# Kernel tuning notes

Measured on AMD Instinct MI355X. Metric: run time of the kernel, lower is better.

Reference implementation:

```python
import jax, jax.numpy as jnp
import numpy as np

N, B, D, H, E = 1024, 8, 768, 8, 16384
DH = D // H
EPS = 1e-5


def setup_inputs() -> dict:
    key = jax.random.key(0)
    ks = jax.random.split(key, 12)
    s = 0.02
    return {
        "x": jax.random.normal(ks[0], (N, B, D), jnp.float32),
        "edge_index": jax.random.randint(ks[1], (B, 2, E), 0, N, jnp.int32),
        "gcn_W": jax.random.normal(ks[2], (D, D), jnp.float32) * s,
        "gcn_b": jnp.zeros((D,), jnp.float32),
        "in_proj_w": jax.random.normal(ks[3], (3 * D, D), jnp.float32) * s,
        "in_proj_b": jnp.zeros((3 * D,), jnp.float32),
        "out_proj_w": jax.random.normal(ks[4], (D, D), jnp.float32) * s,
        "out_proj_b": jnp.zeros((D,), jnp.float32),
        "gate_w": jax.random.normal(ks[5], (D, 2 * D), jnp.float32) * s,
        "gate_b": jnp.zeros((D,), jnp.float32),
        "ln_g": jnp.ones((D,), jnp.float32),
        "ln_b": jnp.zeros((D,), jnp.float32),
    }


def _gcn(xb, edge_index, gcn_W, gcn_b):
    # xb: [B, N, D] node features; edge_index: [B, 2, E]
    h = xb @ gcn_W.T  # linear first, as in PyG GCNConv
    loops = jnp.arange(N, dtype=edge_index.dtype)

    def agg(h_b, ei_b):
        src = jnp.concatenate([ei_b[0], loops])  # add self-loops
        dst = jnp.concatenate([ei_b[1], loops])
        deg = jax.ops.segment_sum(jnp.ones_like(src, h_b.dtype), dst, num_segments=N)
        dinv = jnp.where(deg > 0, jax.lax.rsqrt(deg), 0.0)
        norm = dinv[src] * dinv[dst]  # symmetric normalization
        msg = norm[:, None] * h_b[src]
        return jax.ops.segment_sum(msg, dst, num_segments=N)

    return jax.vmap(agg)(h, edge_index) + gcn_b  # [B, N, D]


def _mha(x, in_proj_w, in_proj_b, out_proj_w, out_proj_b):
    # x: [N, B, D] (seq-first, as nn.MultiheadAttention default)
    qkv = x @ in_proj_w.T + in_proj_b  # [N, B, 3D]
    q, k, v = jnp.split(qkv, 3, axis=-1)

    def heads(t):  # [N, B, D] -> [B, H, N, DH]
        return t.reshape(N, B, H, DH).transpose(1, 2, 0, 3)

    q, k, v = heads(q), heads(k), heads(v)
    scores = jnp.einsum("bhqd,bhkd->bhqk", q, k) / jnp.sqrt(jnp.float32(DH))
    attn = jax.nn.softmax(scores, axis=-1)
    ctx = jnp.einsum("bhqk,bhkd->bhqd", attn, v)  # [B, H, N, DH]
    ctx = ctx.transpose(2, 0, 1, 3).reshape(N, B, D)
    return ctx @ out_proj_w.T + out_proj_b


def _layernorm(x, g, b):
    mu = jnp.mean(x, axis=-1, keepdims=True)
    var = jnp.mean(jnp.square(x - mu), axis=-1, keepdims=True)
    return (x - mu) * jax.lax.rsqrt(var + EPS) * g + b


def reference(x, edge_index, gcn_W, gcn_b, in_proj_w, in_proj_b,
              out_proj_w, out_proj_b, gate_w, gate_b, ln_g, ln_b):
    xb = x.transpose(1, 0, 2)  # [B, N, D]
    gcn_out = _gcn(xb, edge_index, gcn_W, gcn_b).transpose(1, 0, 2)  # [N, B, D]
    attn_out = _mha(x, in_proj_w, in_proj_b, out_proj_w, out_proj_b)  # [N, B, D]
    combined = jnp.concatenate([gcn_out, attn_out], axis=-1)
    gate = jax.nn.sigmoid(combined @ gate_w.T + gate_b)
    fused = gate * gcn_out + (1.0 - gate) * attn_out
    return _layernorm(fused + x, ln_g, ln_b)
```

## Files before the change

kernel.cpp:

```cpp
#include <hip/hip_runtime.h>


typedef __attribute__((ext_vector_type(8))) short b16x8;
typedef __attribute__((ext_vector_type(4))) float f32x4;

using gu32 = __attribute__((address_space(1))) const unsigned int;
using lu32 = __attribute__((address_space(3))) unsigned int;

constexpr int N  = 1024;
constexpr int B  = 8;
constexpr int D  = 768;
constexpr int H  = 8;
constexpr int DH = 96;
constexpr int E  = 16384;
constexpr int M  = N * B;
constexpr float LN_EPS = 1e-5f;

#define DEV static __device__ __forceinline__
#define GLOAD(SRC, DST) __builtin_amdgcn_global_load_lds((gu32*)(SRC), (lu32*)(DST), 16, 0, 0)

DEV unsigned short f2b(float f) {
  unsigned u = __float_as_uint(f);
  u += 0x7fffu + ((u >> 16) & 1u);
  return (unsigned short)(u >> 16);
}
DEV float b2f(unsigned short h) { return __uint_as_float(((unsigned)h) << 16); }

constexpr int CS0 = 1572864;
constexpr int CS1 = CS0 + 147456;
constexpr int CS2 = CS1 + 442368;
constexpr int CS3 = CS2 + 147456;
constexpr int CS4 = CS3 + 294912;
constexpr int CAST_BLOCKS = CS4 / 256;
constexpr int CNT_BLOCKS  = (B * E) / 256;
__global__ void cast_count_kernel(
    const float* __restrict__ x, const float* __restrict__ gcnW,
    const float* __restrict__ ipw, const float* __restrict__ opw,
    const float* __restrict__ gw,
    unsigned short* __restrict__ xb16, unsigned short* __restrict__ wcat,
    unsigned short* __restrict__ wout, unsigned short* __restrict__ wgate,
    const int* __restrict__ ei, int* __restrict__ cnt) {
  const int blk = blockIdx.x;
  if (blk < CAST_BLOCKS) {
    const int i = blk * 256 + threadIdx.x;
    const float* in; unsigned short* out; int off;
    if (i < CS0)      { in = x;    out = xb16;           off = i; }
    else if (i < CS1) { in = gcnW; out = wcat;           off = i - CS0; }
    else if (i < CS2) { in = ipw;  out = wcat + 589824;  off = i - CS1; }
    else if (i < CS3) { in = opw;  out = wout;           off = i - CS2; }
    else              { in = gw;   out = wgate;          off = i - CS3; }
    float4 v = ((const float4*)in)[off];
    ushort4 o;
    o.x = f2b(v.x); o.y = f2b(v.y); o.z = f2b(v.z); o.w = f2b(v.w);
    ((ushort4*)out)[off] = o;
  } else {
    const int j = (blk - CAST_BLOCKS) * 256 + threadIdx.x;
    const int b = j >> 14, e = j & (E - 1);
    const int dst = ei[(b << 15) + E + e];
    atomicAdd(&cnt[(b << 10) + dst], 1);
  }
}

__global__ __launch_bounds__(1024) void scan_offs_kernel(
    const int* __restrict__ cnt, int* __restrict__ offs,
    int* __restrict__ cursor, float* __restrict__ dinv) {
  __shared__ int buf[1024];
  const int b = blockIdx.x, i = threadIdx.x, g = (b << 10) + i;
  const int c = cnt[g];
  buf[i] = c;
  __syncthreads();
  for (int off = 1; off < 1024; off <<= 1) {
    int t = (i >= off) ? buf[i - off] : 0;
    __syncthreads();
    buf[i] += t;
    __syncthreads();
  }
  const int excl = buf[i] - c;
  offs[g] = excl;
  cursor[g] = excl;
  dinv[g] = rsqrtf((float)(c + 1));
}

__global__ void edge_fill_kernel(const int* __restrict__ ei,
                                 int* __restrict__ cursor, int* __restrict__ elist) {
  int i = blockIdx.x * 256 + threadIdx.x;
  int b = i >> 14, e = i & (E - 1);
  int src = ei[(b << 15) + e];
  int dst = ei[(b << 15) + E + e];
  int slot = atomicAdd(&cursor[(b << 10) + dst], 1);
  elist[(b << 14) + slot] = src;
}

constexpr int EPI_FUSED = 0;
constexpr int EPI_ATTN  = 1;
constexpr int EPI_GATE  = 2;

template <int EPI, int BN, int K, int GX, int GY>
__global__ __launch_bounds__(256) void gemm_bt(
    const unsigned short* __restrict__ A, const unsigned short* __restrict__ W,
    const float* __restrict__ bias,
    void* __restrict__ p0, void* __restrict__ p1, void* __restrict__ p2,
    void* __restrict__ p3) {
  constexpr int NW = BN / 32;
  constexpr int NT = K / 32;
  __shared__ __align__(16) unsigned short sA[2][128][32];
  __shared__ __align__(16) unsigned short sB[2][BN][32];
  const int tid = threadIdx.x;
  const int lane = tid & 63, wid = tid >> 6;
  const int wm = wid >> 1, wn = wid & 1;
  const int bid = blockIdx.x;
  const int xcd = bid & 7, slot = bid >> 3;
  const int by = xcd * (GY / 8) + slot / GX;
  const int bx = slot % GX;
  const int m0 = by * 128, n0 = bx * BN;
  const int l15 = lane & 15, lhi = lane >> 4;
  const int srow = lane >> 2;
  const int scol = (((lane & 3) ^ ((lane >> 3) & 3))) * 8;
  const int rcol = ((lhi ^ ((l15 >> 1) & 3))) * 8;

  f32x4 acc[4][NW] = {};

  const unsigned short* pa = A + ((size_t)(m0 + wid * 32 + srow)) * K + scol;
  const unsigned short* pb = W + ((size_t)(n0 + wid * (BN / 4) + srow)) * K + scol;

  auto stage = [&](int buf) {
    GLOAD(pa,          &sA[buf][wid * 32][0]);
    GLOAD(pa + 16 * K, &sA[buf][wid * 32 + 16][0]);
    GLOAD(pb,          &sB[buf][wid * (BN / 4)][0]);
    if constexpr (BN == 128) GLOAD(pb + 16 * K, &sB[buf][wid * 32 + 16][0]);
    pa += 32; pb += 32;
  };

  stage(0);
  int cur = 0;
  for (int kt = 0; kt < NT; ++kt) {
    if (kt + 1 < NT) {
      stage(cur ^ 1);
      if constexpr (BN == 128) asm volatile("s_waitcnt vmcnt(4)" ::: "memory");
      else                     asm volatile("s_waitcnt vmcnt(3)" ::: "memory");
    } else {
      asm volatile("s_waitcnt vmcnt(0)" ::: "memory");
    }
    __builtin_amdgcn_s_barrier();
    __builtin_amdgcn_sched_barrier(0);

    b16x8 af[4], bfr[NW];
#pragma unroll
    for (int i = 0; i < 4; ++i)
      af[i] = *(const b16x8*)&sA[cur][wm * 64 + i * 16 + l15][rcol];
#pragma unroll
    for (int j = 0; j < NW; ++j)
      bfr[j] = *(const b16x8*)&sB[cur][wn * (BN / 2) + j * 16 + l15][rcol];
#pragma unroll
    for (int i = 0; i < 4; ++i)
#pragma unroll
      for (int j = 0; j < NW; ++j)
        acc[i][j] = __builtin_amdgcn_mfma_f32_16x16x32_bf16(af[i], bfr[j], acc[i][j], 0, 0, 0);

    __builtin_amdgcn_sched_barrier(0);
    __builtin_amdgcn_s_barrier();
    cur ^= 1;
  }

#pragma unroll
  for (int i = 0; i < 4; ++i) {
#pragma unroll
    for (int j = 0; j < NW; ++j) {
      const int c = n0 + wn * (BN / 2) + j * 16 + l15;
      float bv;
      if constexpr (EPI == EPI_FUSED) bv = (c < 768) ? 0.0f : bias[c - 768];
      else bv = bias[c];
#pragma unroll
      for (int g = 0; g < 4; ++g) {
        const int r = m0 + wm * 64 + i * 16 + lhi * 4 + g;
        float v = acc[i][j][g] + bv;
        if constexpr (EPI == EPI_FUSED) {
          const int n = r >> 3, b = r & 7;
          if (c < 768) {
            ((unsigned short*)p0)[((size_t)((b << 10) + n)) * 768 + c] = f2b(v);
          } else {
            const int cc2 = c - 768;
            const int sec = cc2 / 768, cc = cc2 - sec * 768;
            const int hd = cc / 96, dh = cc - hd * 96;
            unsigned short* dst =
                (sec == 0) ? (unsigned short*)p1
                           : (sec == 1 ? (unsigned short*)p2 : (unsigned short*)p3);
            size_t idx;
            if (sec < 2) idx = ((size_t)((b * 8 + hd) * 1024 + n)) * 96 + dh;
            else         idx = ((size_t)((b * 8 + hd) * 96 + dh)) * 1024 + n;
            dst[idx] = f2b(v);
          }
        } else if constexpr (EPI == EPI_ATTN) {
          ((unsigned short*)p0)[(size_t)r * 1536 + 768 + c] = f2b(v);
        } else {
          ((unsigned short*)p0)[(size_t)r * 768 + c] =
              f2b(1.0f / (1.0f + __expf(-v)));
        }
      }
    }
  }
}

__global__ __launch_bounds__(256) void attn_agg_kernel(
    const unsigned short* __restrict__ qb, const unsigned short* __restrict__ kb,
    const unsigned short* __restrict__ vb, unsigned short* __restrict__ ctx,
    const unsigned short* __restrict__ h16,
    const int* __restrict__ cnt, const int* __restrict__ offs,
    const int* __restrict__ elist, const float* __restrict__ dinv,
    const float* __restrict__ gcn_b, unsigned short* __restrict__ cat16) {
  __shared__ __align__(16) unsigned short sK[64][104];
  __shared__ __align__(16) unsigned short sV[96][72];
  __shared__ __align__(16) unsigned short sP[4][16][72];

  if (blockIdx.x >= 1024) {
    if (threadIdx.x >= 192) return;
    const int abid = blockIdx.x - 1024;
    const int b = abid & 7, n = abid >> 3;
    const int bn = (b << 10) + n;
    const int d = threadIdx.x * 4;
    const float dn = dinv[bn];
    const size_t hrow = (size_t)bn * 768;
    ushort4 hv = *(const ushort4*)(h16 + hrow + d);
    float a0 = dn * dn * b2f(hv.x), a1 = dn * dn * b2f(hv.y);
    float a2 = dn * dn * b2f(hv.z), a3 = dn * dn * b2f(hv.w);
    const int st = offs[bn], cv = cnt[bn];
    const int* ep = elist + (b << 14) + st;
    int i = 0;
    for (; i + 2 <= cv; i += 2) {
      const int s0 = ep[i], s1 = ep[i + 1];
      const float nv0 = dinv[(b << 10) + s0] * dn;
      const float nv1 = dinv[(b << 10) + s1] * dn;
      const ushort4 r0 = *(const ushort4*)(h16 + ((size_t)((b << 10) + s0)) * 768 + d);
      const ushort4 r1 = *(const ushort4*)(h16 + ((size_t)((b << 10) + s1)) * 768 + d);
      a0 += nv0 * b2f(r0.x) + nv1 * b2f(r1.x);
      a1 += nv0 * b2f(r0.y) + nv1 * b2f(r1.y);
      a2 += nv0 * b2f(r0.z) + nv1 * b2f(r1.z);
      a3 += nv0 * b2f(r0.w) + nv1 * b2f(r1.w);
    }
    if (i < cv) {
      const int s0 = ep[i];
      const float nv0 = dinv[(b << 10) + s0] * dn;
      const ushort4 r0 = *(const ushort4*)(h16 + ((size_t)((b << 10) + s0)) * 768 + d);
      a0 += nv0 * b2f(r0.x); a1 += nv0 * b2f(r0.y);
      a2 += nv0 * b2f(r0.z); a3 += nv0 * b2f(r0.w);
    }
    const float4 bb = *(const float4*)(gcn_b + d);
    a0 += bb.x; a1 += bb.y; a2 += bb.z; a3 += bb.w;
    const size_t crow = ((size_t)n * 8 + b) * 1536;
    ushort4 co; co.x = f2b(a0); co.y = f2b(a1); co.z = f2b(a2); co.w = f2b(a3);
    *(ushort4*)(cat16 + crow + d) = co;
    return;
  }

  const int tid = threadIdx.x, lane = tid & 63, wid = tid >> 6;
  const int l15 = lane & 15, lhi = lane >> 4;
  const int bid = blockIdx.x;
  const int xcd = bid & 7, slot = bid >> 3;
  const int bh = xcd * 8 + (slot >> 4);
  const int q0 = (slot & 15) * 64;
  const float SCL = 0.14724445f;

  b16x8 qf[3];
  const size_t qbase = ((size_t)bh * 1024 + q0 + wid * 16 + l15) * 96 + lhi * 8;
#pragma unroll
  for (int ks = 0; ks < 3; ++ks) qf[ks] = *(const b16x8*)(qb + qbase + ks * 32);

  const int c0 = tid, c1 = 256 + tid, c2 = 512 + tid;
  const unsigned short* kp0 = kb + ((size_t)bh * 1024 + c0 / 12) * 96 + (c0 % 12) * 8;
  const unsigned short* kp1 = kb + ((size_t)bh * 1024 + c1 / 12) * 96 + (c1 % 12) * 8;
  const unsigned short* kp2 = kb + ((size_t)bh * 1024 + c2 / 12) * 96 + (c2 % 12) * 8;
  const unsigned short* vp0 = vb + ((size_t)bh * 96 + (c0 >> 3)) * 1024 + (c0 & 7) * 8;
  const unsigned short* vp1 = vb + ((size_t)bh * 96 + (c1 >> 3)) * 1024 + (c1 & 7) * 8;
  const unsigned short* vp2 = vb + ((size_t)bh * 96 + (c2 >> 3)) * 1024 + (c2 & 7) * 8;
  unsigned short* sk0 = &sK[c0 / 12][(c0 % 12) * 8];
  unsigned short* sk1 = &sK[c1 / 12][(c1 % 12) * 8];
  unsigned short* sk2 = &sK[c2 / 12][(c2 % 12) * 8];
  unsigned short* sv0 = &sV[c0 >> 3][(c0 & 7) * 8];
  unsigned short* sv1 = &sV[c1 >> 3][(c1 & 7) * 8];
  unsigned short* sv2 = &sV[c2 >> 3][(c2 & 7) * 8];

  uint4 k0 = *(const uint4*)kp0, k1 = *(const uint4*)kp1, k2 = *(const uint4*)kp2;
  uint4 v0 = *(const uint4*)vp0, v1 = *(const uint4*)vp1, v2 = *(const uint4*)vp2;

  f32x4 accO[6] = {};
  float ssum[4] = {0.f, 0.f, 0.f, 0.f};

  for (int kt = 0; kt < 16; ++kt) {
    __syncthreads();
    *(uint4*)sk0 = k0; *(uint4*)sk1 = k1; *(uint4*)sk2 = k2;
    *(uint4*)sv0 = v0; *(uint4*)sv1 = v1; *(uint4*)sv2 = v2;
    __syncthreads();
    if (kt < 15) {
      kp0 += 64 * 96; kp1 += 64 * 96; kp2 += 64 * 96;
      vp0 += 64;      vp1 += 64;      vp2 += 64;
      k0 = *(const uint4*)kp0; k1 = *(const uint4*)kp1; k2 = *(const uint4*)kp2;
      v0 = *(const uint4*)vp0; v1 = *(const uint4*)vp1; v2 = *(const uint4*)vp2;
    }

    f32x4 sf[4] = {};
    __builtin_amdgcn_s_setprio(1);
#pragma unroll
    for (int f = 0; f < 4; ++f) {
#pragma unroll
      for (int ks = 0; ks < 3; ++ks) {
        b16x8 kf = *(const b16x8*)&sK[f * 16 + l15][ks * 32 + lhi * 8];
        sf[f] = __builtin_amdgcn_mfma_f32_16x16x32_bf16(qf[ks], kf, sf[f], 0, 0, 0);
      }
    }
    __builtin_amdgcn_s_setprio(0);

#pragma unroll
    for (int g = 0; g < 4; ++g) {
#pragma unroll
      for (int f = 0; f < 4; ++f) {
        const float pv = exp2f(sf[f][g] * SCL);
        sP[wid][lhi * 4 + g][f * 16 + l15] = f2b(pv);
        ssum[g] += pv;
      }
    }

    __builtin_amdgcn_s_setprio(1);
#pragma unroll
    for (int ks = 0; ks < 2; ++ks) {
      b16x8 pa = *(const b16x8*)&sP[wid][l15][ks * 32 + lhi * 8];
#pragma unroll
      for (int o = 0; o < 6; ++o) {
        b16x8 vf = *(const b16x8*)&sV[o * 16 + l15][ks * 32 + lhi * 8];
        accO[o] = __builtin_amdgcn_mfma_f32_16x16x32_bf16(pa, vf, accO[o], 0, 0, 0);
      }
    }
    __builtin_amdgcn_s_setprio(0);
  }

#pragma unroll
  for (int g = 0; g < 4; ++g) {
#pragma unroll
    for (int msk = 1; msk < 16; msk <<= 1) ssum[g] += __shfl_xor(ssum[g], msk);
  }

  const int b = bh >> 3, hd = bh & 7;
  float rinv[4];
#pragma unroll
  for (int g = 0; g < 4; ++g) rinv[g] = 1.0f / ssum[g];
#pragma unroll
  for (int o = 0; o < 6; ++o)
#pragma unroll
    for (int g = 0; g < 4; ++g) {
      const int qrow = q0 + wid * 16 + lhi * 4 + g;
      ctx[((size_t)qrow * 8 + b) * 768 + hd * 96 + o * 16 + l15] =
          f2b(accO[o][g] * rinv[g]);
    }
}

__global__ __launch_bounds__(192) void ln_fuse_kernel(
    const unsigned short* __restrict__ gate16,
    const unsigned short* __restrict__ cat16,
    const float* __restrict__ x,
    const float* __restrict__ lng, const float* __restrict__ lnb,
    float* __restrict__ out) {
  const int r = blockIdx.x;
  const int t = threadIdx.x, lane = t & 63, wid = t >> 6;
  const int d = t * 4;
  const size_t xrow = (size_t)r * 768;
  const size_t crow = (size_t)r * 1536;
  const ushort4 gv = *(const ushort4*)(gate16 + xrow + d);
  const ushort4 cv = *(const ushort4*)(cat16 + crow + d);
  const ushort4 av = *(const ushort4*)(cat16 + crow + 768 + d);
  const float4 xv = *(const float4*)(x + xrow + d);
  const float g0 = b2f(gv.x), g1 = b2f(gv.y), g2 = b2f(gv.z), g3 = b2f(gv.w);
  float f0 = g0 * b2f(cv.x) + (1.f - g0) * b2f(av.x) + xv.x;
  float f1 = g1 * b2f(cv.y) + (1.f - g1) * b2f(av.y) + xv.y;
  float f2 = g2 * b2f(cv.z) + (1.f - g2) * b2f(av.z) + xv.z;
  float f3 = g3 * b2f(cv.w) + (1.f - g3) * b2f(av.w) + xv.w;
  float s1 = f0 + f1 + f2 + f3;
  float s2 = f0 * f0 + f1 * f1 + f2 * f2 + f3 * f3;
#pragma unroll
  for (int msk = 1; msk < 64; msk <<= 1) {
    s1 += __shfl_xor(s1, msk);
    s2 += __shfl_xor(s2, msk);
  }
  __shared__ float p1[3], p2[3];
  if (lane == 0) { p1[wid] = s1; p2[wid] = s2; }
  __syncthreads();
  s1 = p1[0] + p1[1] + p1[2];
  s2 = p2[0] + p2[1] + p2[2];
  const float mu = s1 * (1.f / 768.f);
  float var = s2 * (1.f / 768.f) - mu * mu;
  var = fmaxf(var, 0.f);
  const float rstd = rsqrtf(var + LN_EPS);
  const float4 lg = *(const float4*)(lng + d);
  const float4 lb = *(const float4*)(lnb + d);
  float4 o;
  o.x = (f0 - mu) * rstd * lg.x + lb.x;
  o.y = (f1 - mu) * rstd * lg.y + lb.y;
  o.z = (f2 - mu) * rstd * lg.z + lb.z;
  o.w = (f3 - mu) * rstd * lg.w + lb.w;
  *(float4*)(out + xrow + d) = o;
}

extern "C" void kernel_launch(void* const* d_in, const int* in_sizes, int n_in,
                              void* d_out, int out_size, void* d_ws, size_t ws_size,
                              hipStream_t stream) {
  const float* x     = (const float*)d_in[0];
  const int*   ei    = (const int*)d_in[1];
  const float* gcnW  = (const float*)d_in[2];
  const float* gcnb  = (const float*)d_in[3];
  const float* ipw   = (const float*)d_in[4];
  const float* ipb   = (const float*)d_in[5];
  const float* opw   = (const float*)d_in[6];
  const float* opb   = (const float*)d_in[7];
  const float* gw    = (const float*)d_in[8];
  const float* gb    = (const float*)d_in[9];
  const float* lng   = (const float*)d_in[10];
  const float* lnb   = (const float*)d_in[11];
  float* out = (float*)d_out;

  char* p = (char*)d_ws;
  auto alloc = [&](size_t bytes) { void* q = p; p += (bytes + 255) & ~(size_t)255; return q; };

  unsigned short* xb16  = (unsigned short*)alloc((size_t)M * 768 * 2);
  unsigned short* wcat  = (unsigned short*)alloc((size_t)3072 * 768 * 2);
  unsigned short* wout  = (unsigned short*)alloc((size_t)768 * 768 * 2);
  unsigned short* wgate = (unsigned short*)alloc((size_t)768 * 1536 * 2);
  unsigned short* qb    = (unsigned short*)alloc((size_t)B * H * N * DH * 2);
  unsigned short* kb    = (unsigned short*)alloc((size_t)B * H * N * DH * 2);
  unsigned short* vb    = (unsigned short*)alloc((size_t)B * H * DH * N * 2);
  unsigned short* h16   = (unsigned short*)alloc((size_t)M * 768 * 2);
  unsigned short* cat16 = (unsigned short*)alloc((size_t)M * 1536 * 2);
  int* cnt    = (int*)alloc(8192 * 4);
  int* offs   = (int*)alloc(8192 * 4);
  int* cursor = (int*)alloc(8192 * 4);
  float* dinv = (float*)alloc(8192 * 4);
  int* elist  = (int*)alloc((size_t)B * E * 4);

  unsigned short* ctx16  = xb16;
  unsigned short* gate16 = qb;

  hipMemsetAsync(cnt, 0, 8192 * 4, stream);
  cast_count_kernel<<<CAST_BLOCKS + CNT_BLOCKS, 256, 0, stream>>>(
      x, gcnW, ipw, opw, gw, xb16, wcat, wout, wgate, ei, cnt);

  scan_offs_kernel<<<8, 1024, 0, stream>>>(cnt, offs, cursor, dinv);
  edge_fill_kernel<<<(B * E) / 256, 256, 0, stream>>>(ei, cursor, elist);

  gemm_bt<EPI_FUSED, 128, 768, 24, 64><<<1536, 256, 0, stream>>>(
      xb16, wcat, ipb, (void*)h16, (void*)qb, (void*)kb, (void*)vb);
  attn_agg_kernel<<<1024 + 8192, 256, 0, stream>>>(
      qb, kb, vb, ctx16, h16, cnt, offs, elist, dinv, gcnb, cat16);
  gemm_bt<EPI_ATTN, 64, 768, 12, 64><<<768, 256, 0, stream>>>(
      ctx16, wout, opb, (void*)cat16, nullptr, nullptr, nullptr);
  gemm_bt<EPI_GATE, 64, 1536, 12, 64><<<768, 256, 0, stream>>>(
      cat16, wgate, gb, (void*)gate16, nullptr, nullptr, nullptr);

  ln_fuse_kernel<<<8192, 192, 0, stream>>>(gate16, cat16, x, lng, lnb, out);
}
```

Measured before the change: 256.6 us.

## Fold out-projection into gate weights and run out-proj and gate GEMMs concurrently

The gate GEMM's attention half is rewritten algebraically: W_gate2·(ctx·Wout^T + b_out) becomes ctx·(W_gate2·Wout)^T plus a precomputed fused bias. The folded weight is computed inside the QKV GEMM launch, which removes the data dependency between the out-projection and gate GEMMs so both run in one launch. The edge-scan and edge-fill kernels are also merged into one, using shared-memory atomics for the cursor. In exchange it adds an extra small weight GEMM, a strided transpose write, and a second rounding to bf16 on the folded weights, which can shift precision slightly.

```diff
diff --git a/kernel.cpp b/kernel.cpp
--- a/kernel.cpp
+++ b/kernel.cpp
@@ -36,35 +36,73 @@
 __global__ void cast_count_kernel(
     const float* __restrict__ x, const float* __restrict__ gcnW,
     const float* __restrict__ ipw, const float* __restrict__ opw,
-    const float* __restrict__ gw,
+    const float* __restrict__ gw, const float* __restrict__ opb,
+    const float* __restrict__ gb,
     unsigned short* __restrict__ xb16, unsigned short* __restrict__ wcat,
-    unsigned short* __restrict__ wout, unsigned short* __restrict__ wgate,
+    unsigned short* __restrict__ wout, unsigned short* __restrict__ woutT,
+    unsigned short* __restrict__ wg2, unsigned short* __restrict__ w2buf,
+    float* __restrict__ bias_fuse,
     const int* __restrict__ ei, int* __restrict__ cnt) {
   const int blk = blockIdx.x;
   if (blk < CAST_BLOCKS) {
     const int i = blk * 256 + threadIdx.x;
-    const float* in; unsigned short* out; int off;
-    if (i < CS0)      { in = x;    out = xb16;           off = i; }
-    else if (i < CS1) { in = gcnW; out = wcat;           off = i - CS0; }
-    else if (i < CS2) { in = ipw;  out = wcat + 589824;  off = i - CS1; }
-    else if (i < CS3) { in = opw;  out = wout;           off = i - CS2; }
-    else              { in = gw;   out = wgate;          off = i - CS3; }
-    float4 v = ((const float4*)in)[off];
-    ushort4 o;
-    o.x = f2b(v.x); o.y = f2b(v.y); o.z = f2b(v.z); o.w = f2b(v.w);
-    ((ushort4*)out)[off] = o;
-  } else {
+    if (i < CS0) {
+      float4 v = ((const float4*)x)[i];
+      ushort4 o; o.x = f2b(v.x); o.y = f2b(v.y); o.z = f2b(v.z); o.w = f2b(v.w);
+      ((ushort4*)xb16)[i] = o;
+    } else if (i < CS1) {
+      const int off = i - CS0;
+      float4 v = ((const float4*)gcnW)[off];
+      ushort4 o; o.x = f2b(v.x); o.y = f2b(v.y); o.z = f2b(v.z); o.w = f2b(v.w);
+      ((ushort4*)wcat)[off] = o;
+    } else if (i < CS2) {
+      const int off = i - CS1;
+      float4 v = ((const float4*)ipw)[off];
+      ushort4 o; o.x = f2b(v.x); o.y = f2b(v.y); o.z = f2b(v.z); o.w = f2b(v.w);
+      ((ushort4*)(wcat + 589824))[off] = o;
+    } else if (i < CS3) {
+      const int off = i - CS2;
+      float4 v = ((const float4*)opw)[off];
+      ushort4 o; o.x = f2b(v.x); o.y = f2b(v.y); o.z = f2b(v.z); o.w = f2b(v.w);
+      ((ushort4*)wout)[off] = o;
+      const int e = off * 4, t = e / 768, j = e % 768;
+      woutT[(size_t)(j + 0) * 768 + t] = o.x;
+      woutT[(size_t)(j + 1) * 768 + t] = o.y;
+      woutT[(size_t)(j + 2) * 768 + t] = o.z;
+      woutT[(size_t)(j + 3) * 768 + t] = o.w;
+    } else {
+      const int off = i - CS3;
+      float4 v = ((const float4*)gw)[off];
+      ushort4 o; o.x = f2b(v.x); o.y = f2b(v.y); o.z = f2b(v.z); o.w = f2b(v.w);
+      const int e = off * 4, c = e / 1536, k = e % 1536;
+      if (k < 768) *(ushort4*)(wg2 + (size_t)c * 1536 + k) = o;
+      else         *(ushort4*)(w2buf + (size_t)c * 768 + (k - 768)) = o;
+    }
+  } else if (blk < CAST_BLOCKS + CNT_BLOCKS) {
     const int j = (blk - CAST_BLOCKS) * 256 + threadIdx.x;
     const int b = j >> 14, e = j & (E - 1);
     const int dst = ei[(b << 15) + E + e];
     atomicAdd(&cnt[(b << 10) + dst], 1);
-  }
-}
-
-__global__ __launch_bounds__(1024) void scan_offs_kernel(
+  } else {
+    const int c = (blk - CAST_BLOCKS - CNT_BLOCKS) * 256 + threadIdx.x;
+    float acc = gb[c];
+    const float* wrow = gw + (size_t)c * 1536 + 768;
+#pragma unroll 4
+    for (int t = 0; t < 768; t += 4) {
+      const float4 wv = *(const float4*)(wrow + t);
+      const float4 bv = *(const float4*)(opb + t);
+      acc += wv.x * bv.x + wv.y * bv.y + wv.z * bv.z + wv.w * bv.w;
+    }
+    bias_fuse[c] = acc;
+  }
+}
+
+__global__ __launch_bounds__(1024) void scan_fill_kernel(
     const int* __restrict__ cnt, int* __restrict__ offs,
-    int* __restrict__ cursor, float* __restrict__ dinv) {
+    float* __restrict__ dinv, const int* __restrict__ ei,
+    int* __restrict__ elist) {
   __shared__ int buf[1024];
+  __shared__ int cur[1024];
   const int b = blockIdx.x, i = threadIdx.x, g = (b << 10) + i;
   const int c = cnt[g];
   buf[i] = c;
@@ -77,42 +115,34 @@
   }
   const int excl = buf[i] - c;
   offs[g] = excl;
-  cursor[g] = excl;
   dinv[g] = rsqrtf((float)(c + 1));
-}
-
-__global__ void edge_fill_kernel(const int* __restrict__ ei,
-                                 int* __restrict__ cursor, int* __restrict__ elist) {
-  int i = blockIdx.x * 256 + threadIdx.x;
-  int b = i >> 14, e = i & (E - 1);
-  int src = ei[(b << 15) + e];
-  int dst = ei[(b << 15) + E + e];
-  int slot = atomicAdd(&cursor[(b << 10) + dst], 1);
-  elist[(b << 14) + slot] = src;
+  cur[i] = excl;
+  __syncthreads();
+  for (int e = i; e < E; e += 1024) {
+    const int src = ei[(b << 15) + e];
+    const int dst = ei[(b << 15) + E + e];
+    const int slot = atomicAdd(&cur[dst], 1);
+    elist[(b << 14) + slot] = src;
+  }
 }
 
 constexpr int EPI_FUSED = 0;
-constexpr int EPI_ATTN  = 1;
-constexpr int EPI_GATE  = 2;
-
-template <int EPI, int BN, int K, int GX, int GY>
-__global__ __launch_bounds__(256) void gemm_bt(
-    const unsigned short* __restrict__ A, const unsigned short* __restrict__ W,
-    const float* __restrict__ bias,
-    void* __restrict__ p0, void* __restrict__ p1, void* __restrict__ p2,
-    void* __restrict__ p3) {
+constexpr int EPI_WF    = 1;
+constexpr int EPI_OUT   = 2;
+constexpr int EPI_GATE  = 3;
+
+template <int EPI, int BN, int K, int LDA>
+DEV void gemm_body(const unsigned short* __restrict__ A,
+                   const unsigned short* __restrict__ W,
+                   const float* __restrict__ bias, int m0, int n0,
+                   void* __restrict__ p0, void* __restrict__ p1,
+                   void* __restrict__ p2, void* __restrict__ p3,
+                   unsigned short* sAp, unsigned short* sBp) {
   constexpr int NW = BN / 32;
   constexpr int NT = K / 32;
-  __shared__ __align__(16) unsigned short sA[2][128][32];
-  __shared__ __align__(16) unsigned short sB[2][BN][32];
   const int tid = threadIdx.x;
   const int lane = tid & 63, wid = tid >> 6;
   const int wm = wid >> 1, wn = wid & 1;
-  const int bid = blockIdx.x;
-  const int xcd = bid & 7, slot = bid >> 3;
-  const int by = xcd * (GY / 8) + slot / GX;
-  const int bx = slot % GX;
-  const int m0 = by * 128, n0 = bx * BN;
   const int l15 = lane & 15, lhi = lane >> 4;
   const int srow = lane >> 2;
   const int scol = (((lane & 3) ^ ((lane >> 3) & 3))) * 8;
@@ -120,14 +150,15 @@
 
   f32x4 acc[4][NW] = {};
 
-  const unsigned short* pa = A + ((size_t)(m0 + wid * 32 + srow)) * K + scol;
+  const unsigned short* pa = A + ((size_t)(m0 + wid * 32 + srow)) * LDA + scol;
   const unsigned short* pb = W + ((size_t)(n0 + wid * (BN / 4) + srow)) * K + scol;
 
   auto stage = [&](int buf) {
-    GLOAD(pa,          &sA[buf][wid * 32][0]);
-    GLOAD(pa + 16 * K, &sA[buf][wid * 32 + 16][0]);
-    GLOAD(pb,          &sB[buf][wid * (BN / 4)][0]);
-    if constexpr (BN == 128) GLOAD(pb + 16 * K, &sB[buf][wid * 32 + 16][0]);
+    GLOAD(pa,            sAp + (buf * 128 + wid * 32) * 32);
+    GLOAD(pa + 16 * LDA, sAp + (buf * 128 + wid * 32 + 16) * 32);
+    GLOAD(pb,            sBp + (buf * BN + wid * (BN / 4)) * 32);
+    if constexpr (BN == 128)
+      GLOAD(pb + 16 * K, sBp + (buf * BN + wid * 32 + 16) * 32);
     pa += 32; pb += 32;
   };
 
@@ -147,10 +178,10 @@
     b16x8 af[4], bfr[NW];
 #pragma unroll
     for (int i = 0; i < 4; ++i)
-      af[i] = *(const b16x8*)&sA[cur][wm * 64 + i * 16 + l15][rcol];
+      af[i] = *(const b16x8*)(sAp + (cur * 128 + wm * 64 + i * 16 + l15) * 32 + rcol);
 #pragma unroll
     for (int j = 0; j < NW; ++j)
-      bfr[j] = *(const b16x8*)&sB[cur][wn * (BN / 2) + j * 16 + l15][rcol];
+      bfr[j] = *(const b16x8*)(sBp + (cur * BN + wn * (BN / 2) + j * 16 + l15) * 32 + rcol);
 #pragma unroll
     for (int i = 0; i < 4; ++i)
 #pragma unroll
@@ -169,6 +200,7 @@
       const int c = n0 + wn * (BN / 2) + j * 16 + l15;
       float bv;
       if constexpr (EPI == EPI_FUSED) bv = (c < 768) ? 0.0f : bias[c - 768];
+      else if constexpr (EPI == EPI_WF) bv = 0.0f;
       else bv = bias[c];
 #pragma unroll
       for (int g = 0; g < 4; ++g) {
@@ -190,8 +222,10 @@
             else         idx = ((size_t)((b * 8 + hd) * 96 + dh)) * 1024 + n;
             dst[idx] = f2b(v);
           }
-        } else if constexpr (EPI == EPI_ATTN) {
+        } else if constexpr (EPI == EPI_WF) {
           ((unsigned short*)p0)[(size_t)r * 1536 + 768 + c] = f2b(v);
+        } else if constexpr (EPI == EPI_OUT) {
+          ((unsigned short*)p0)[(size_t)r * 768 + c] = f2b(v);
         } else {
           ((unsigned short*)p0)[(size_t)r * 768 + c] =
               f2b(1.0f / (1.0f + __expf(-v)));
@@ -201,13 +235,58 @@
   }
 }
 
+__global__ __launch_bounds__(256) void gemm_fused_wf(
+    const unsigned short* __restrict__ xb16, const unsigned short* __restrict__ wcat,
+    const float* __restrict__ ipb,
+    unsigned short* __restrict__ h16, unsigned short* __restrict__ qb,
+    unsigned short* __restrict__ kb, unsigned short* __restrict__ vb,
+    const unsigned short* __restrict__ w2buf, const unsigned short* __restrict__ woutT,
+    unsigned short* __restrict__ wg2) {
+  __shared__ __align__(16) unsigned short sAbuf[2 * 128 * 32];
+  __shared__ __align__(16) unsigned short sBbuf[2 * 128 * 32];
+  if (blockIdx.x < 1536) {
+    const int bid = blockIdx.x;
+    const int xcd = bid & 7, slot = bid >> 3;
+    const int m0 = (xcd * 8 + slot / 24) * 128, n0 = (slot % 24) * 128;
+    gemm_body<EPI_FUSED, 128, 768, 768>(xb16, wcat, ipb, m0, n0,
+                                        h16, qb, kb, vb, sAbuf, sBbuf);
+  } else {
+    const int b2 = blockIdx.x - 1536;
+    const int m0 = (b2 / 6) * 128, n0 = (b2 % 6) * 128;
+    gemm_body<EPI_WF, 128, 768, 768>(w2buf, woutT, nullptr, m0, n0,
+                                     wg2, nullptr, nullptr, nullptr, sAbuf, sBbuf);
+  }
+}
+
+__global__ __launch_bounds__(256) void gemm_op_gate(
+    const unsigned short* __restrict__ cat2, const unsigned short* __restrict__ wout,
+    const float* __restrict__ opb, unsigned short* __restrict__ attnf16,
+    const unsigned short* __restrict__ wg2, const float* __restrict__ bias_fuse,
+    unsigned short* __restrict__ gate16) {
+  __shared__ __align__(16) unsigned short sAbuf[2 * 128 * 32];
+  __shared__ __align__(16) unsigned short sBbuf[2 * 64 * 32];
+  if (blockIdx.x < 768) {
+    const int bid = blockIdx.x;
+    const int xcd = bid & 7, slot = bid >> 3;
+    const int m0 = (xcd * 8 + slot / 12) * 128, n0 = (slot % 12) * 64;
+    gemm_body<EPI_OUT, 64, 768, 1536>(cat2 + 768, wout, opb, m0, n0,
+                                      attnf16, nullptr, nullptr, nullptr, sAbuf, sBbuf);
+  } else {
+    const int bid = blockIdx.x - 768;
+    const int xcd = bid & 7, slot = bid >> 3;
+    const int m0 = (xcd * 8 + slot / 12) * 128, n0 = (slot % 12) * 64;
+    gemm_body<EPI_GATE, 64, 1536, 1536>(cat2, wg2, bias_fuse, m0, n0,
+                                        gate16, nullptr, nullptr, nullptr, sAbuf, sBbuf);
+  }
+}
+
 __global__ __launch_bounds__(256) void attn_agg_kernel(
     const unsigned short* __restrict__ qb, const unsigned short* __restrict__ kb,
-    const unsigned short* __restrict__ vb, unsigned short* __restrict__ ctx,
+    const unsigned short* __restrict__ vb, unsigned short* __restrict__ cat2,
     const unsigned short* __restrict__ h16,
     const int* __restrict__ cnt, const int* __restrict__ offs,
     const int* __restrict__ elist, const float* __restrict__ dinv,
-    const float* __restrict__ gcn_b, unsigned short* __restrict__ cat16) {
+    const float* __restrict__ gcn_b) {
   __shared__ __align__(16) unsigned short sK[64][104];
   __shared__ __align__(16) unsigned short sV[96][72];
   __shared__ __align__(16) unsigned short sP[4][16][72];
@@ -248,7 +327,7 @@
     a0 += bb.x; a1 += bb.y; a2 += bb.z; a3 += bb.w;
     const size_t crow = ((size_t)n * 8 + b) * 1536;
     ushort4 co; co.x = f2b(a0); co.y = f2b(a1); co.z = f2b(a2); co.w = f2b(a3);
-    *(ushort4*)(cat16 + crow + d) = co;
+    *(ushort4*)(cat2 + crow + d) = co;
     return;
   }
 
@@ -347,14 +426,15 @@
 #pragma unroll
     for (int g = 0; g < 4; ++g) {
       const int qrow = q0 + wid * 16 + lhi * 4 + g;
-      ctx[((size_t)qrow * 8 + b) * 768 + hd * 96 + o * 16 + l15] =
+      cat2[((size_t)qrow * 8 + b) * 1536 + 768 + hd * 96 + o * 16 + l15] =
           f2b(accO[o][g] * rinv[g]);
     }
 }
 
 __global__ __launch_bounds__(192) void ln_fuse_kernel(
     const unsigned short* __restrict__ gate16,
-    const unsigned short* __restrict__ cat16,
+    const unsigned short* __restrict__ cat2,
+    const unsigned short* __restrict__ attnf16,
     const float* __restrict__ x,
     const float* __restrict__ lng, const float* __restrict__ lnb,
     float* __restrict__ out) {
@@ -364,8 +444,8 @@
   const size_t xrow = (size_t)r * 768;
   const size_t crow = (size_t)r * 1536;
   const ushort4 gv = *(const ushort4*)(gate16 + xrow + d);
-  const ushort4 cv = *(const ushort4*)(cat16 + crow + d);
-  const ushort4 av = *(const ushort4*)(cat16 + crow + 768 + d);
+  const ushort4 cv = *(const ushort4*)(cat2 + crow + d);
+  const ushort4 av = *(const ushort4*)(attnf16 + xrow + d);
   const float4 xv = *(const float4*)(x + xrow + d);
   const float g0 = b2f(gv.x), g1 = b2f(gv.y), g2 = b2f(gv.z), g3 = b2f(gv.w);
   float f0 = g0 * b2f(cv.x) + (1.f - g0) * b2f(av.x) + xv.x;
@@ -421,36 +501,36 @@
   unsigned short* xb16  = (unsigned short*)alloc((size_t)M * 768 * 2);
   unsigned short* wcat  = (unsigned short*)alloc((size_t)3072 * 768 * 2);
   unsigned short* wout  = (unsigned short*)alloc((size_t)768 * 768 * 2);
-  unsigned short* wgate = (unsigned short*)alloc((size_t)768 * 1536 * 2);
+  unsigned short* woutT = (unsigned short*)alloc((size_t)768 * 768 * 2);
+  unsigned short* w2buf = (unsigned short*)alloc((size_t)768 * 768 * 2);
+  unsigned short* wg2   = (unsigned short*)alloc((size_t)768 * 1536 * 2);
   unsigned short* qb    = (unsigned short*)alloc((size_t)B * H * N * DH * 2);
   unsigned short* kb    = (unsigned short*)alloc((size_t)B * H * N * DH * 2);
   unsigned short* vb    = (unsigned short*)alloc((size_t)B * H * DH * N * 2);
   unsigned short* h16   = (unsigned short*)alloc((size_t)M * 768 * 2);
-  unsigned short* cat16 = (unsigned short*)alloc((size_t)M * 1536 * 2);
+  unsigned short* cat2  = (unsigned short*)alloc((size_t)M * 1536 * 2);
+  float* bias_fuse      = (float*)alloc(768 * 4);
   int* cnt    = (int*)alloc(8192 * 4);
   int* offs   = (int*)alloc(8192 * 4);
-  int* cursor = (int*)alloc(8192 * 4);
   float* dinv = (float*)alloc(8192 * 4);
   int* elist  = (int*)alloc((size_t)B * E * 4);
 
-  unsigned short* ctx16  = xb16;
-  unsigned short* gate16 = qb;
+  unsigned short* gate16  = qb;
+  unsigned short* attnf16 = kb;
 
   hipMemsetAsync(cnt, 0, 8192 * 4, stream);
-  cast_count_kernel<<<CAST_BLOCKS + CNT_BLOCKS, 256, 0, stream>>>(
-      x, gcnW, ipw, opw, gw, xb16, wcat, wout, wgate, ei, cnt);
-
-  scan_offs_kernel<<<8, 1024, 0, stream>>>(cnt, offs, cursor, dinv);
-  edge_fill_kernel<<<(B * E) / 256, 256, 0, stream>>>(ei, cursor, elist);
-
-  gemm_bt<EPI_FUSED, 128, 768, 24, 64><<<1536, 256, 0, stream>>>(
-      xb16, wcat, ipb, (void*)h16, (void*)qb, (void*)kb, (void*)vb);
+  cast_count_kernel<<<CAST_BLOCKS + CNT_BLOCKS + 3, 256, 0, stream>>>(
+      x, gcnW, ipw, opw, gw, opb, gb,
+      xb16, wcat, wout, woutT, wg2, w2buf, bias_fuse, ei, cnt);
+
+  scan_fill_kernel<<<8, 1024, 0, stream>>>(cnt, offs, dinv, ei, elist);
+
+  gemm_fused_wf<<<1536 + 36, 256, 0, stream>>>(
+      xb16, wcat, ipb, h16, qb, kb, vb, w2buf, woutT, wg2);
   attn_agg_kernel<<<1024 + 8192, 256, 0, stream>>>(
-      qb, kb, vb, ctx16, h16, cnt, offs, elist, dinv, gcnb, cat16);
-  gemm_bt<EPI_ATTN, 64, 768, 12, 64><<<768, 256, 0, stream>>>(
-      ctx16, wout, opb, (void*)cat16, nullptr, nullptr, nullptr);
-  gemm_bt<EPI_GATE, 64, 1536, 12, 64><<<768, 256, 0, stream>>>(
-      cat16, wgate, gb, (void*)gate16, nullptr, nullptr, nullptr);
-
-  ln_fuse_kernel<<<8192, 192, 0, stream>>>(gate16, cat16, x, lng, lnb, out);
-}
+      qb, kb, vb, cat2, h16, cnt, offs, elist, dinv, gcnb);
+  gemm_op_gate<<<1536, 256, 0, stream>>>(
+      cat2, wout, opb, attnf16, wg2, bias_fuse, gate16);
+
+  ln_fuse_kernel<<<8192, 192, 0, stream>>>(gate16, cat2, attnf16, x, lng, lnb, out);
+}
```

Result: slower. 293.4 us (+14.3%).
